# Optimization experiments

Measured on AMD Instinct MI355X. Metric: run time of the kernel, lower is better.

## Reference

```python
import jax, jax.numpy as jnp
import numpy as np

B, S, H, C = 2, 128, 768, 5
NEG = -1024.0

def setup_inputs() -> dict:
    key = jax.random.key(0)
    ks = jax.random.split(key, 6)
    sequence_output = jax.random.normal(ks[0], (B, S, H), dtype=jnp.float32)
    attention_mask = jnp.ones((B, S), dtype=jnp.int32)
    ng_token_mask = jax.random.bernoulli(ks[1], 0.5, (B, S, C, S))  # bool
    target = (jax.random.uniform(ks[2], (B, S, C, S)) < 0.01).astype(jnp.float32)
    lim = 1.0 / np.sqrt(H)
    W_prd = jax.random.uniform(ks[3], (H, H), jnp.float32, -lim, lim)
    b_prd = jnp.zeros((H,), jnp.float32)
    W_arg = jax.random.uniform(ks[4], (C * H, H), jnp.float32, -lim, lim)
    b_arg = jnp.zeros((C * H,), jnp.float32)
    W_out = jax.random.uniform(ks[5], (C, H), jnp.float32, -lim, lim)
    return dict(sequence_output=sequence_output, attention_mask=attention_mask,
                ng_token_mask=ng_token_mask, target=target,
                W_prd=W_prd, b_prd=b_prd, W_arg=W_arg, b_arg=b_arg, W_out=W_out)

def reference(sequence_output, attention_mask, ng_token_mask, target,
              W_prd, b_prd, W_arg, b_arg, W_out):
    b, s, h = sequence_output.shape
    c = W_out.shape[0]
    # get_mask: ng mask restricted to attended tokens, then any over case dim
    mask = ng_token_mask & (attention_mask[:, None, None, :] > 0)   # (B,S,C,S)
    mask = jnp.any(mask, axis=2, keepdims=True)                      # (B,S,1,S)
    # dropout is identity in eval mode
    h_p = sequence_output @ W_prd.T + b_prd                          # (B,S,H)
    h_a = (sequence_output @ W_arg.T + b_arg).reshape(b, s, c, h)    # (B,S,C,H)
    # outer-sum biaffine: (B, S_prd, S_arg, C, H)
    hh = jnp.tanh(h_p[:, :, None, None, :] + h_a[:, None, :, :, :])
    # per-case Linear(H,1,bias=False), stacked at dim=2 -> (B, S_prd, C, S_arg)
    output = jnp.einsum('bpach,ch->bpca', hh, W_out)
    output = output + (~mask).astype(output.dtype) * NEG
    # cross_entropy_pas_loss: multi-hot CE over candidate (last) axis
    log_sm = jax.nn.log_softmax(output, axis=3)
    loss = jnp.sum(-log_sm * target) / jnp.sum(target)
    return loss, output
```

## Files before the change

kernel.cpp:

```cpp
#include <hip/hip_runtime.h>
#include <math.h>

#define Bb 2
#define Ss 128
#define Hh 768
#define Cc 5
#define Mm 256
#define NEGV -1024.0f
#define SCALE 2.8853900817779268f

#define PT 2
#define NBLK (Mm / PT * Cc)

typedef __attribute__((ext_vector_type(8))) short bf16x8;
typedef __attribute__((ext_vector_type(4))) float f32x4;
typedef unsigned short ushort;

__device__ __forceinline__ unsigned pack_hi16(float hi, float lo) {
    return (__float_as_uint(hi) & 0xFFFF0000u) | (__float_as_uint(lo) >> 16);
}
__device__ __forceinline__ bf16x8 pack_bf16x8(float4 lo, float4 hi) {
    union { bf16x8 v; unsigned u[4]; } r;
    r.u[0] = pack_hi16(lo.y, lo.x);
    r.u[1] = pack_hi16(lo.w, lo.z);
    r.u[2] = pack_hi16(hi.y, hi.x);
    r.u[3] = pack_hi16(hi.w, hi.z);
    return r.v;
}

#define SB __builtin_amdgcn_sched_barrier(0);

__global__ __launch_bounds__(256)
void gemm_mfma(const float* __restrict__ X,
               const float* __restrict__ Wprd,
               const float* __restrict__ Warg,
               const float* __restrict__ bprd,
               const float* __restrict__ barg,
               float* __restrict__ hp_out,
               ushort* __restrict__ haTb,
               float* __restrict__ accum)
{
    __shared__ __align__(16) ushort Asb[64][40];
    __shared__ __align__(16) ushort Bsb[32][40];

    if (blockIdx.x == 0 && blockIdx.y == 0 && threadIdx.x == 0) {
        accum[0] = 0.f; accum[1] = 0.f;
        ((unsigned*)accum)[2] = 0u;
    }
    const int bm   = blockIdx.x;
    const int bn   = blockIdx.y;
    const int tid  = threadIdx.x;
    const int wave = tid >> 6;
    const int lane = tid & 63;
    const int l16  = lane & 15;
    const int quad = lane >> 4;

    const float* Wsrc; const float* bsrc;
    const int nb = bn * 32;
    if (nb < Hh) { Wsrc = Wprd + (size_t)nb * Hh;        bsrc = bprd + nb; }
    else         { Wsrc = Warg + (size_t)(nb - Hh) * Hh; bsrc = barg + (nb - Hh); }

    const int srow = tid >> 2;
    const int sko  = (tid & 3) * 8;
    const float* gA = X + (size_t)(bm * 64 + srow) * Hh + sko;
    const float* gB = Wsrc + (size_t)(tid >> 2) * Hh + sko;

    float4 pa0 = *(const float4*)(gA);
    float4 pa1 = *(const float4*)(gA + 4);
    float4 pb0, pb1;
    if (tid < 128) { pb0 = *(const float4*)(gB); pb1 = *(const float4*)(gB + 4); }

    f32x4 acc0 = {0.f,0.f,0.f,0.f}, acc1 = {0.f,0.f,0.f,0.f};

    for (int k0 = 0; k0 < Hh; k0 += 32) {
        *(bf16x8*)&Asb[srow][sko] = pack_bf16x8(pa0, pa1);
        if (tid < 128) *(bf16x8*)&Bsb[tid >> 2][sko] = pack_bf16x8(pb0, pb1);
        __syncthreads();
        const int kn = k0 + 32;
        if (kn < Hh) {
            pa0 = *(const float4*)(gA + kn);
            pa1 = *(const float4*)(gA + kn + 4);
            if (tid < 128) { pb0 = *(const float4*)(gB + kn); pb1 = *(const float4*)(gB + kn + 4); }
        }
        bf16x8 af = *(const bf16x8*)&Asb[wave * 16 + l16][quad * 8];
        bf16x8 b0 = *(const bf16x8*)&Bsb[l16][quad * 8];
        bf16x8 b1 = *(const bf16x8*)&Bsb[16 + l16][quad * 8];
        acc0 = __builtin_amdgcn_mfma_f32_16x16x32_bf16(af, b0, acc0, 0, 0, 0);
        acc1 = __builtin_amdgcn_mfma_f32_16x16x32_bf16(af, b1, acc1, 0, 0, 0);
        __syncthreads();
    }

    const float sb0 = SCALE * bsrc[l16];
    const float sb1 = SCALE * bsrc[16 + l16];
    const int row = bm * 64 + wave * 16 + quad * 4;

    if (nb < Hh) {
        #pragma unroll
        for (int r = 0; r < 4; ++r) {
            const int mm = row + r;
            hp_out[(size_t)mm * Hh + nb + l16]      = SCALE * acc0[r] + sb0;
            hp_out[(size_t)mm * Hh + nb + 16 + l16] = SCALE * acc1[r] + sb1;
        }
    } else {
        const int q  = nb - Hh;
        const int cU = q / Hh;
        const int h0 = q % Hh;
        const int hA = h0 + l16;
        const int hB = h0 + 16 + l16;
        const size_t offA = (size_t)(hA >> 3) * 1024 + (hA & 7);
        const size_t offB = (size_t)(hB >> 3) * 1024 + (hB & 7);
        #pragma unroll
        for (int r = 0; r < 4; ++r) {
            const int mm = row + r;
            const int bI = mm >> 7, aI = mm & 127;
            const size_t base = ((size_t)(bI * Cc + cU) * 96) * 1024 + (size_t)aI * 8;
            const float v0 = SCALE * acc0[r] + sb0;
            const float v1 = SCALE * acc1[r] + sb1;
            haTb[base + offA] = (ushort)(__float_as_uint(v0) >> 16);
            haTb[base + offB] = (ushort)(__float_as_uint(v1) >> 16);
        }
    }
}

#define LOADG4(R, g) \
    R##0 = hap4[((g)*4+0)*128]; R##1 = hap4[((g)*4+1)*128]; \
    R##2 = hap4[((g)*4+2)*128]; R##3 = hap4[((g)*4+3)*128];

#define C1(u, hx) { \
    const float e0 = __builtin_amdgcn_exp2f(__uint_as_float((u).x << 16)); \
    const float e1 = __builtin_amdgcn_exp2f(__uint_as_float((u).x & 0xFFFF0000u)); \
    const float e2 = __builtin_amdgcn_exp2f(__uint_as_float((u).y << 16)); \
    const float e3 = __builtin_amdgcn_exp2f(__uint_as_float((u).y & 0xFFFF0000u)); \
    const float e4 = __builtin_amdgcn_exp2f(__uint_as_float((u).z << 16)); \
    const float e5 = __builtin_amdgcn_exp2f(__uint_as_float((u).z & 0xFFFF0000u)); \
    const float e6 = __builtin_amdgcn_exp2f(__uint_as_float((u).w << 16)); \
    const float e7 = __builtin_amdgcn_exp2f(__uint_as_float((u).w & 0xFFFF0000u)); \
    const float4 wA  = *(const float4*)(wc_s + (hx)); \
    const float4 wB  = *(const float4*)(wc_s + (hx) + 4); \
    const float4 p0A = *(const float4*)(&Eps[0][hx]); \
    const float4 p0B = *(const float4*)(&Eps[0][(hx) + 4]); \
    const float4 p1A = *(const float4*)(&Eps[1][hx]); \
    const float4 p1B = *(const float4*)(&Eps[1][(hx) + 4]); \
    float r; \
    r = __builtin_amdgcn_rcpf(fmaf(p0A.x, e0, 1.0f)); ac00 = fmaf(wA.x, r, ac00); \
    r = __builtin_amdgcn_rcpf(fmaf(p0A.y, e1, 1.0f)); ac01 = fmaf(wA.y, r, ac01); \
    r = __builtin_amdgcn_rcpf(fmaf(p0A.z, e2, 1.0f)); ac00 = fmaf(wA.z, r, ac00); \
    r = __builtin_amdgcn_rcpf(fmaf(p0A.w, e3, 1.0f)); ac01 = fmaf(wA.w, r, ac01); \
    r = __builtin_amdgcn_rcpf(fmaf(p0B.x, e4, 1.0f)); ac00 = fmaf(wB.x, r, ac00); \
    r = __builtin_amdgcn_rcpf(fmaf(p0B.y, e5, 1.0f)); ac01 = fmaf(wB.y, r, ac01); \
    r = __builtin_amdgcn_rcpf(fmaf(p0B.z, e6, 1.0f)); ac00 = fmaf(wB.z, r, ac00); \
    r = __builtin_amdgcn_rcpf(fmaf(p0B.w, e7, 1.0f)); ac01 = fmaf(wB.w, r, ac01); \
    r = __builtin_amdgcn_rcpf(fmaf(p1A.x, e0, 1.0f)); ac10 = fmaf(wA.x, r, ac10); \
    r = __builtin_amdgcn_rcpf(fmaf(p1A.y, e1, 1.0f)); ac11 = fmaf(wA.y, r, ac11); \
    r = __builtin_amdgcn_rcpf(fmaf(p1A.z, e2, 1.0f)); ac10 = fmaf(wA.z, r, ac10); \
    r = __builtin_amdgcn_rcpf(fmaf(p1A.w, e3, 1.0f)); ac11 = fmaf(wA.w, r, ac11); \
    r = __builtin_amdgcn_rcpf(fmaf(p1B.x, e4, 1.0f)); ac10 = fmaf(wB.x, r, ac10); \
    r = __builtin_amdgcn_rcpf(fmaf(p1B.y, e5, 1.0f)); ac11 = fmaf(wB.y, r, ac11); \
    r = __builtin_amdgcn_rcpf(fmaf(p1B.z, e6, 1.0f)); ac10 = fmaf(wB.z, r, ac10); \
    r = __builtin_amdgcn_rcpf(fmaf(p1B.w, e7, 1.0f)); ac11 = fmaf(wB.w, r, ac11); \
}

#define CONSUMEG4(R, g) \
    C1(R##0, hbase + ((g)*4+0)*8)  C1(R##1, hbase + ((g)*4+1)*8) \
    C1(R##2, hbase + ((g)*4+2)*8)  C1(R##3, hbase + ((g)*4+3)*8)

__global__ __launch_bounds__(512, 6)
void biaffine_loss(const float* __restrict__ hp_all,
                   const ushort* __restrict__ haTb,
                   const float* __restrict__ Wout,
                   const int* __restrict__ ng,
                   const int* __restrict__ att,
                   const float* __restrict__ target,
                   float* __restrict__ out_logits,
                   float* __restrict__ accum,
                   float* __restrict__ out_loss)
{
    __shared__ float Eps[PT][Hh];
    __shared__ float wc_s[Hh];
    __shared__ float partial[PT][3][Ss];
    __shared__ float maskneg[PT][Ss];
    __shared__ float redmax[PT][2];
    __shared__ float red3[PT][2][3];
    __shared__ float swr_s;

    const int pt  = blockIdx.x / Cc;
    const int c   = blockIdx.x - pt * Cc;
    const int bp0 = pt * PT;
    const int b   = bp0 >> 7;
    const int tid = threadIdx.x;
    const int a   = tid & (Ss - 1);
    const int hq  = tid >> 7;
    const int lane = tid & 63;

    for (int i = tid; i < PT * Hh; i += 512)
        ((float*)Eps)[i] = __builtin_amdgcn_exp2f(hp_all[(size_t)bp0 * Hh + i]);
    for (int i = tid; i < Hh; i += 512)      wc_s[i] = Wout[(size_t)c * Hh + i];
    if (tid < PT * Ss) {
        const int p_i = tid >> 7;
        const int aa  = tid & (Ss - 1);
        int any = 0;
        if (att[b * Ss + aa] > 0) {
            const int* ngp = ng + (size_t)(bp0 + p_i) * Cc * Ss + aa;
            #pragma unroll
            for (int cc = 0; cc < Cc; ++cc) any |= ngp[cc * Ss];
        }
        maskneg[p_i][aa] = any ? 0.0f : NEGV;
    }
    __syncthreads();

    if (tid < 64) {
        float s = 0.f;
        #pragma unroll
        for (int i = 0; i < Hh / 64; ++i) s += wc_s[tid + i * 64];
        #pragma unroll
        for (int off = 32; off; off >>= 1) s += __shfl_xor(s, off, 64);
        if (tid == 0) swr_s = s;
    }

    const uint4* hap4 = (const uint4*)(haTb + ((size_t)(b * Cc + c) * 96) * 1024)
                      + (size_t)hq * 24 * 128 + a;
    const int hbase = hq * 192;

    uint4 A0, A1, A2, A3;
    uint4 B0, B1, B2, B3;
    float ac00 = 0.f, ac01 = 0.f, ac10 = 0.f, ac11 = 0.f;

    LOADG4(A, 0) SB
    LOADG4(B, 1) SB  CONSUMEG4(A, 0) SB
    LOADG4(A, 2) SB  CONSUMEG4(B, 1) SB
    LOADG4(B, 3) SB  CONSUMEG4(A, 2) SB
    LOADG4(A, 4) SB  CONSUMEG4(B, 3) SB
    LOADG4(B, 5) SB  CONSUMEG4(A, 4) SB
    CONSUMEG4(B, 5)

    if (hq != 0) {
        partial[0][hq - 1][a] = ac00 + ac01;
        partial[1][hq - 1][a] = ac10 + ac11;
    }
    __syncthreads();

    float logit[PT];
    const int wv = tid >> 6;
    if (hq == 0) {
        const float ps[PT] = { ac00 + ac01, ac10 + ac11 };
        #pragma unroll
        for (int p = 0; p < PT; ++p) {
            const float full = ps[p] + partial[p][0][a] + partial[p][1][a] + partial[p][2][a];
            logit[p] = swr_s - 2.0f * full + maskneg[p][a];
            out_logits[((size_t)(bp0 + p) * Cc + c) * Ss + a] = logit[p];
            float mx = logit[p];
            #pragma unroll
            for (int off = 32; off; off >>= 1) mx = fmaxf(mx, __shfl_xor(mx, off, 64));
            if (lane == 0) redmax[p][wv] = mx;
        }
    }
    __syncthreads();

    if (hq == 0) {
        #pragma unroll
        for (int p = 0; p < PT; ++p) {
            const float rm = fmaxf(redmax[p][0], redmax[p][1]);
            const float e  = __builtin_amdgcn_exp2f((logit[p] - rm) * 1.4426950408889634f);
            const float tg = target[((size_t)(bp0 + p) * Cc + c) * Ss + a];
            float se = e, st = tg, sx = tg * logit[p];
            #pragma unroll
            for (int off = 32; off; off >>= 1) {
                se += __shfl_xor(se, off, 64);
                st += __shfl_xor(st, off, 64);
                sx += __shfl_xor(sx, off, 64);
            }
            if (lane == 0) { red3[p][wv][0] = se; red3[p][wv][1] = st; red3[p][wv][2] = sx; }
        }
    }
    __syncthreads();

    if (tid == 0) {
        float nsum = 0.f, dsum = 0.f;
        #pragma unroll
        for (int p = 0; p < PT; ++p) {
            const float rm = fmaxf(redmax[p][0], redmax[p][1]);
            const float SE = red3[p][0][0] + red3[p][1][0];
            const float ST = red3[p][0][1] + red3[p][1][1];
            const float SX = red3[p][0][2] + red3[p][1][2];
            const float lse = rm + __builtin_amdgcn_logf(SE) * 0.6931471805599453f;
            nsum += lse * ST - SX;
            dsum += ST;
        }
        atomicAdd(&accum[0], nsum);
        atomicAdd(&accum[1], dsum);
        __threadfence();
        const unsigned old = atomicAdd((unsigned*)(accum + 2), 1u);
        if (old == (unsigned)(NBLK - 1)) {
            const float n = atomicAdd(&accum[0], 0.0f);
            const float d = atomicAdd(&accum[1], 0.0f);
            out_loss[0] = n / d;
        }
    }
}

extern "C" void kernel_launch(void* const* d_in, const int* in_sizes, int n_in,
                              void* d_out, int out_size, void* d_ws, size_t ws_size,
                              hipStream_t stream) {
    const float* seq    = (const float*)d_in[0];
    const int*   att    = (const int*)  d_in[1];
    const int*   ng     = (const int*)  d_in[2];
    const float* target = (const float*)d_in[3];
    const float* Wprd   = (const float*)d_in[4];
    const float* bprd   = (const float*)d_in[5];
    const float* Warg   = (const float*)d_in[6];
    const float* barg   = (const float*)d_in[7];
    const float* Wout   = (const float*)d_in[8];

    float*  out    = (float*)d_out;
    float*  hp_out = (float*)d_ws;
    ushort* haTb   = (ushort*)(hp_out + 196608);
    float*  accum  = hp_out + 196608 + 491520;

    gemm_mfma<<<dim3(4, 144), 256, 0, stream>>>(seq, Wprd, Warg, bprd, barg,
                                                hp_out, haTb, accum);
    biaffine_loss<<<dim3(NBLK), 512, 0, stream>>>(hp_out, haTb, Wout, ng, att, target,
                                                  out + 1, accum, out);
}
```

Baseline: 134.2 us.

## Precompute exp of predicate projection in GEMM and read weights via scalar loads

The GEMM epilogue now writes exp2 of the scaled predicate projection, so the biaffine kernel no longer applies exp per block. The biaffine kernel drops its shared-memory staging of Eps and Wout and the barrier that followed it. It reads these values directly from global memory through wave-uniform pointers (hq is made uniform with readfirstlane) so they can become scalar or broadcast loads. This cuts shared-memory traffic and a sync, and may raise occupancy, at the cost of relying on cache hits for repeated global reads.

```diff
diff --git a/kernel.cpp b/kernel.cpp
--- a/kernel.cpp
+++ b/kernel.cpp
@@ -36,7 +36,7 @@
                const float* __restrict__ Warg,
                const float* __restrict__ bprd,
                const float* __restrict__ barg,
-               float* __restrict__ hp_out,
+               float* __restrict__ EpG,
                ushort* __restrict__ haTb,
                float* __restrict__ accum)
 {
@@ -98,8 +98,8 @@
         #pragma unroll
         for (int r = 0; r < 4; ++r) {
             const int mm = row + r;
-            hp_out[(size_t)mm * Hh + nb + l16]      = SCALE * acc0[r] + sb0;
-            hp_out[(size_t)mm * Hh + nb + 16 + l16] = SCALE * acc1[r] + sb1;
+            EpG[(size_t)mm * Hh + nb + l16]      = __builtin_amdgcn_exp2f(SCALE * acc0[r] + sb0);
+            EpG[(size_t)mm * Hh + nb + 16 + l16] = __builtin_amdgcn_exp2f(SCALE * acc1[r] + sb1);
         }
     } else {
         const int q  = nb - Hh;
@@ -127,6 +127,11 @@
     R##2 = hap4[((g)*4+2)*128]; R##3 = hap4[((g)*4+3)*128];
 
 #define C1(u, hx) { \
+    float w8[8], q0[8], q1[8]; \
+    _Pragma("unroll") \
+    for (int z = 0; z < 8; ++z) { \
+        w8[z] = wrow[(hx) + z]; q0[z] = ep0[(hx) + z]; q1[z] = ep1[(hx) + z]; \
+    } \
     const float e0 = __builtin_amdgcn_exp2f(__uint_as_float((u).x << 16)); \
     const float e1 = __builtin_amdgcn_exp2f(__uint_as_float((u).x & 0xFFFF0000u)); \
     const float e2 = __builtin_amdgcn_exp2f(__uint_as_float((u).y << 16)); \
@@ -135,29 +140,23 @@
     const float e5 = __builtin_amdgcn_exp2f(__uint_as_float((u).z & 0xFFFF0000u)); \
     const float e6 = __builtin_amdgcn_exp2f(__uint_as_float((u).w << 16)); \
     const float e7 = __builtin_amdgcn_exp2f(__uint_as_float((u).w & 0xFFFF0000u)); \
-    const float4 wA  = *(const float4*)(wc_s + (hx)); \
-    const float4 wB  = *(const float4*)(wc_s + (hx) + 4); \
-    const float4 p0A = *(const float4*)(&Eps[0][hx]); \
-    const float4 p0B = *(const float4*)(&Eps[0][(hx) + 4]); \
-    const float4 p1A = *(const float4*)(&Eps[1][hx]); \
-    const float4 p1B = *(const float4*)(&Eps[1][(hx) + 4]); \
     float r; \
-    r = __builtin_amdgcn_rcpf(fmaf(p0A.x, e0, 1.0f)); ac00 = fmaf(wA.x, r, ac00); \
-    r = __builtin_amdgcn_rcpf(fmaf(p0A.y, e1, 1.0f)); ac01 = fmaf(wA.y, r, ac01); \
-    r = __builtin_amdgcn_rcpf(fmaf(p0A.z, e2, 1.0f)); ac00 = fmaf(wA.z, r, ac00); \
-    r = __builtin_amdgcn_rcpf(fmaf(p0A.w, e3, 1.0f)); ac01 = fmaf(wA.w, r, ac01); \
-    r = __builtin_amdgcn_rcpf(fmaf(p0B.x, e4, 1.0f)); ac00 = fmaf(wB.x, r, ac00); \
-    r = __builtin_amdgcn_rcpf(fmaf(p0B.y, e5, 1.0f)); ac01 = fmaf(wB.y, r, ac01); \
-    r = __builtin_amdgcn_rcpf(fmaf(p0B.z, e6, 1.0f)); ac00 = fmaf(wB.z, r, ac00); \
-    r = __builtin_amdgcn_rcpf(fmaf(p0B.w, e7, 1.0f)); ac01 = fmaf(wB.w, r, ac01); \
-    r = __builtin_amdgcn_rcpf(fmaf(p1A.x, e0, 1.0f)); ac10 = fmaf(wA.x, r, ac10); \
-    r = __builtin_amdgcn_rcpf(fmaf(p1A.y, e1, 1.0f)); ac11 = fmaf(wA.y, r, ac11); \
-    r = __builtin_amdgcn_rcpf(fmaf(p1A.z, e2, 1.0f)); ac10 = fmaf(wA.z, r, ac10); \
-    r = __builtin_amdgcn_rcpf(fmaf(p1A.w, e3, 1.0f)); ac11 = fmaf(wA.w, r, ac11); \
-    r = __builtin_amdgcn_rcpf(fmaf(p1B.x, e4, 1.0f)); ac10 = fmaf(wB.x, r, ac10); \
-    r = __builtin_amdgcn_rcpf(fmaf(p1B.y, e5, 1.0f)); ac11 = fmaf(wB.y, r, ac11); \
-    r = __builtin_amdgcn_rcpf(fmaf(p1B.z, e6, 1.0f)); ac10 = fmaf(wB.z, r, ac10); \
-    r = __builtin_amdgcn_rcpf(fmaf(p1B.w, e7, 1.0f)); ac11 = fmaf(wB.w, r, ac11); \
+    r = __builtin_amdgcn_rcpf(fmaf(q0[0], e0, 1.0f)); ac00 = fmaf(w8[0], r, ac00); \
+    r = __builtin_amdgcn_rcpf(fmaf(q0[1], e1, 1.0f)); ac01 = fmaf(w8[1], r, ac01); \
+    r = __builtin_amdgcn_rcpf(fmaf(q0[2], e2, 1.0f)); ac00 = fmaf(w8[2], r, ac00); \
+    r = __builtin_amdgcn_rcpf(fmaf(q0[3], e3, 1.0f)); ac01 = fmaf(w8[3], r, ac01); \
+    r = __builtin_amdgcn_rcpf(fmaf(q0[4], e4, 1.0f)); ac00 = fmaf(w8[4], r, ac00); \
+    r = __builtin_amdgcn_rcpf(fmaf(q0[5], e5, 1.0f)); ac01 = fmaf(w8[5], r, ac01); \
+    r = __builtin_amdgcn_rcpf(fmaf(q0[6], e6, 1.0f)); ac00 = fmaf(w8[6], r, ac00); \
+    r = __builtin_amdgcn_rcpf(fmaf(q0[7], e7, 1.0f)); ac01 = fmaf(w8[7], r, ac01); \
+    r = __builtin_amdgcn_rcpf(fmaf(q1[0], e0, 1.0f)); ac10 = fmaf(w8[0], r, ac10); \
+    r = __builtin_amdgcn_rcpf(fmaf(q1[1], e1, 1.0f)); ac11 = fmaf(w8[1], r, ac11); \
+    r = __builtin_amdgcn_rcpf(fmaf(q1[2], e2, 1.0f)); ac10 = fmaf(w8[2], r, ac10); \
+    r = __builtin_amdgcn_rcpf(fmaf(q1[3], e3, 1.0f)); ac11 = fmaf(w8[3], r, ac11); \
+    r = __builtin_amdgcn_rcpf(fmaf(q1[4], e4, 1.0f)); ac10 = fmaf(w8[4], r, ac10); \
+    r = __builtin_amdgcn_rcpf(fmaf(q1[5], e5, 1.0f)); ac11 = fmaf(w8[5], r, ac11); \
+    r = __builtin_amdgcn_rcpf(fmaf(q1[6], e6, 1.0f)); ac10 = fmaf(w8[6], r, ac10); \
+    r = __builtin_amdgcn_rcpf(fmaf(q1[7], e7, 1.0f)); ac11 = fmaf(w8[7], r, ac11); \
 }
 
 #define CONSUMEG4(R, g) \
@@ -165,7 +164,7 @@
     C1(R##2, hbase + ((g)*4+2)*8)  C1(R##3, hbase + ((g)*4+3)*8)
 
 __global__ __launch_bounds__(512, 6)
-void biaffine_loss(const float* __restrict__ hp_all,
+void biaffine_loss(const float* __restrict__ EpG,
                    const ushort* __restrict__ haTb,
                    const float* __restrict__ Wout,
                    const int* __restrict__ ng,
@@ -175,8 +174,6 @@
                    float* __restrict__ accum,
                    float* __restrict__ out_loss)
 {
-    __shared__ float Eps[PT][Hh];
-    __shared__ float wc_s[Hh];
     __shared__ float partial[PT][3][Ss];
     __shared__ float maskneg[PT][Ss];
     __shared__ float redmax[PT][2];
@@ -189,12 +186,13 @@
     const int b   = bp0 >> 7;
     const int tid = threadIdx.x;
     const int a   = tid & (Ss - 1);
-    const int hq  = tid >> 7;
+    const int hq  = __builtin_amdgcn_readfirstlane(tid >> 7);
     const int lane = tid & 63;
 
-    for (int i = tid; i < PT * Hh; i += 512)
-        ((float*)Eps)[i] = __builtin_amdgcn_exp2f(hp_all[(size_t)bp0 * Hh + i]);
-    for (int i = tid; i < Hh; i += 512)      wc_s[i] = Wout[(size_t)c * Hh + i];
+    const float* wrow = Wout + (size_t)c * Hh;
+    const float* ep0  = EpG + (size_t)(bp0 + 0) * Hh;
+    const float* ep1  = EpG + (size_t)(bp0 + 1) * Hh;
+
     if (tid < PT * Ss) {
         const int p_i = tid >> 7;
         const int aa  = tid & (Ss - 1);
@@ -206,12 +204,11 @@
         }
         maskneg[p_i][aa] = any ? 0.0f : NEGV;
     }
-    __syncthreads();
 
     if (tid < 64) {
         float s = 0.f;
         #pragma unroll
-        for (int i = 0; i < Hh / 64; ++i) s += wc_s[tid + i * 64];
+        for (int i = 0; i < Hh / 64; ++i) s += wrow[tid + i * 64];
         #pragma unroll
         for (int off = 32; off; off >>= 1) s += __shfl_xor(s, off, 64);
         if (tid == 0) swr_s = s;
@@ -312,12 +309,12 @@
     const float* Wout   = (const float*)d_in[8];
 
     float*  out    = (float*)d_out;
-    float*  hp_out = (float*)d_ws;
-    ushort* haTb   = (ushort*)(hp_out + 196608);
-    float*  accum  = hp_out + 196608 + 491520;
+    float*  EpG    = (float*)d_ws;
+    ushort* haTb   = (ushort*)(EpG + 196608);
+    float*  accum  = EpG + 196608 + 491520;
 
     gemm_mfma<<<dim3(4, 144), 256, 0, stream>>>(seq, Wprd, Warg, bprd, barg,
-                                                hp_out, haTb, accum);
-    biaffine_loss<<<dim3(NBLK), 512, 0, stream>>>(hp_out, haTb, Wout, ng, att, target,
+                                                EpG, haTb, accum);
+    biaffine_loss<<<dim3(NBLK), 512, 0, stream>>>(EpG, haTb, Wout, ng, att, target,
                                                   out + 1, accum, out);
 }
```

Result: no change. 132.1 us (-1.5%).
